# Performance work log

Measured on AMD Instinct MI355X. Metric: run time of the kernel, lower is better.

Reference implementation:

```python
import jax, jax.numpy as jnp
import numpy as np

N = 50000      # nodes
E = 800000     # edges
IN = 128       # in_channels
H = 128        # hidden_channels
OUT = 500      # out_channels
EPS = 1e-5


def setup_inputs() -> dict:
    key = jax.random.key(0)
    ks = jax.random.split(key, 8)
    def rn(k, shape, scale=0.05):
        return jax.random.normal(k, shape, jnp.float32) * scale
    return {
        "x": jax.random.normal(ks[0], (N, IN), jnp.float32),
        "edge_index": jax.random.randint(ks[1], (2, E), 0, N, dtype=jnp.int32),
        "W1": rn(ks[2], (IN, H)), "b1": jnp.zeros((H,), jnp.float32),
        "g1": jnp.ones((H,), jnp.float32), "be1": jnp.zeros((H,), jnp.float32),
        "W2": rn(ks[3], (H, 2 * H)), "b2": jnp.zeros((2 * H,), jnp.float32),
        "g2": jnp.ones((2 * H,), jnp.float32), "be2": jnp.zeros((2 * H,), jnp.float32),
        "W3": rn(ks[4], (2 * H, H)), "b3": jnp.zeros((H,), jnp.float32),
        "g3": jnp.ones((H,), jnp.float32), "be3": jnp.zeros((H,), jnp.float32),
        "Wl1": rn(ks[5], (H, H // 2)), "bl1": jnp.zeros((H // 2,), jnp.float32),
        "g4": jnp.ones((H // 2,), jnp.float32), "be4": jnp.zeros((H // 2,), jnp.float32),
        "Wl2": rn(ks[6], (H // 2, OUT)), "bl2": jnp.zeros((OUT,), jnp.float32),
    }


def layer_norm(x, g, b):
    mu = jnp.mean(x, axis=-1, keepdims=True)
    var = jnp.mean(jnp.square(x - mu), axis=-1, keepdims=True)
    return (x - mu) * jax.lax.rsqrt(var + EPS) * g + b


def gcn_conv(x, W, b, src, dst, n):
    # PyG GCNConv: x' = D^{-1/2} (A + I) D^{-1/2} (x W) + b, with self-loops.
    h = x @ W                                   # [N, F]
    ones = jnp.ones(src.shape[0], h.dtype)
    deg = jax.ops.segment_sum(ones, dst, num_segments=n) + 1.0  # +1 self-loop
    dinv = jnp.where(deg > 0, jax.lax.rsqrt(deg), 0.0)          # [N]
    coef = dinv[src] * dinv[dst]                # [E]
    agg = jax.ops.segment_sum(h[src] * coef[:, None], dst, num_segments=n)
    agg = agg + h * jnp.square(dinv)[:, None]   # self-loop messages
    return agg + b


def reference(x, edge_index, W1, b1, g1, be1, W2, b2, g2, be2,
              W3, b3, g3, be3, Wl1, bl1, g4, be4, Wl2, bl2):
    # eval mode: dropout is identity
    src, dst = edge_index[0], edge_index[1]
    n = x.shape[0]
    h = jax.nn.elu(layer_norm(gcn_conv(x, W1, b1, src, dst, n), g1, be1))
    h = jax.nn.elu(layer_norm(gcn_conv(h, W2, b2, src, dst, n), g2, be2))
    h = jax.nn.elu(layer_norm(gcn_conv(h, W3, b3, src, dst, n), g3, be3))
    h = jax.nn.elu(layer_norm(h @ Wl1 + bl1, g4, be4))
    return h @ Wl2 + bl2
```

## Files before the change

### kernel.cpp

```cpp
#include <hip/hip_runtime.h>
#include <cstdint>


#define LN_EPS 1e-5f

typedef __attribute__((ext_vector_type(8))) short bf16x8;
typedef __attribute__((ext_vector_type(4))) float f32x4;

static __device__ __forceinline__ ushort f2bf(float f) {
  union { float f; uint u; } c; c.f = f;
  uint u = c.u;
  return (ushort)((u + 0x7fffu + ((u >> 16) & 1u)) >> 16);
}
static __device__ __forceinline__ float bf2f(ushort h) {
  union { uint u; float f; } c; c.u = (uint)h << 16;
  return c.f;
}


__global__ void deg_kernel(const int* __restrict__ dst, int* __restrict__ deg, int E) {
  int e = blockIdx.x * blockDim.x + threadIdx.x;
  if (e < E) atomicAdd(&deg[dst[e]], 1);
}

__global__ void scan1_kernel(const int* __restrict__ deg, int* __restrict__ excl,
                             int* __restrict__ bsums, float* __restrict__ dinv, int N) {
  __shared__ int s[256];
  int tid = threadIdx.x;
  int i = blockIdx.x * 256 + tid;
  int v = (i < N) ? deg[i] : 0;
  s[tid] = v;
  __syncthreads();
  for (int o = 1; o < 256; o <<= 1) {
    int t = (tid >= o) ? s[tid - o] : 0;
    __syncthreads();
    if (tid >= o) s[tid] += t;
    __syncthreads();
  }
  if (i < N) {
    excl[i] = s[tid] - v;
    dinv[i] = rsqrtf((float)v + 1.0f);
  }
  if (tid == 255) bsums[blockIdx.x] = s[tid];
}

__global__ void scan23_kernel(int* __restrict__ rowptr, int* __restrict__ fill,
                              const int* __restrict__ bsums, int N, int Etotal, int nb) {
  __shared__ int sh[256];
  const int tid = threadIdx.x;
  const int bix = blockIdx.x;
  int v = (tid < bix && tid < nb) ? bsums[tid] : 0;
  sh[tid] = v;
  __syncthreads();
  for (int o = 128; o > 0; o >>= 1) {
    if (tid < o) sh[tid] += sh[tid + o];
    __syncthreads();
  }
  const int off = sh[0];
  int i = bix * 256 + tid;
  if (i < N) {
    int r = rowptr[i] + off;
    rowptr[i] = r;
    fill[i] = r;
  } else if (i == N) {
    rowptr[N] = Etotal;
  }
}

__global__ void fill_kernel(const int* __restrict__ src, const int* __restrict__ dst,
                            int* __restrict__ fill, int* __restrict__ srcs, int E) {
  int e = blockIdx.x * blockDim.x + threadIdx.x;
  if (e >= E) return;
  int idx = atomicAdd(&fill[dst[e]], 1);
  srcs[idx] = src[e];
}


struct WConvArgs {
  const float* w[5];
  ushort* wt[5];
  int K[5], N[5];
  int off[6];
};

__global__ void prep_kernel(WConvArgs a, int total, int* __restrict__ deg, int Nn) {
  int i = blockIdx.x * blockDim.x + threadIdx.x;
  if (i < Nn) deg[i] = 0;
  if (i >= total) return;
  int m = 0;
  while (i >= a.off[m + 1]) m++;
  int j = i - a.off[m];
  int k = j / a.N[m], n = j - k * a.N[m];
  a.wt[m][(size_t)n * a.K[m] + k] = f2bf(a.w[m][j]);
}

#define TBM 128
#define TBN 128
#define TBK 32
#define LDK 40

template <int AF32, int EMODE>
__global__ __launch_bounds__(256, 2) void mfma_gemm_kernel(
    const void* __restrict__ A, const ushort* __restrict__ Bt,
    const float* __restrict__ bias, const float* __restrict__ gamma,
    const float* __restrict__ beta, void* __restrict__ Cout,
    int M, int N, int K) {
  __shared__ ushort As[TBM][LDK];
  __shared__ ushort Bs[TBN][LDK];
  const int tid = threadIdx.x;
  const int lane = tid & 63;
  const int w = tid >> 6;
  const int wm = w & 1, wn = w >> 1;
  const int quad = lane >> 4, l16 = lane & 15;
  const int rowBase = blockIdx.y * TBM;
  const int colBase = blockIdx.x * TBN;

  f32x4 acc[4][4] = {};
  const int lr = tid >> 2;
  const int lk = (tid & 3) * 8;

  for (int k0 = 0; k0 < K; k0 += TBK) {
#pragma unroll
    for (int h = 0; h < 2; h++) {
      int r = lr + h * 64;
      int grow = rowBase + r;
      if (AF32) {
        const float* Af = (const float*)A;
        float4 v0 = make_float4(0.f, 0.f, 0.f, 0.f), v1 = v0;
        if (grow < M) {
          const float* ap = Af + (size_t)grow * K + k0 + lk;
          v0 = *(const float4*)ap;
          v1 = *(const float4*)(ap + 4);
        }
        uint4 wv;
        wv.x = (uint)f2bf(v0.x) | ((uint)f2bf(v0.y) << 16);
        wv.y = (uint)f2bf(v0.z) | ((uint)f2bf(v0.w) << 16);
        wv.z = (uint)f2bf(v1.x) | ((uint)f2bf(v1.y) << 16);
        wv.w = (uint)f2bf(v1.z) | ((uint)f2bf(v1.w) << 16);
        *(uint4*)&As[r][lk] = wv;
      } else {
        const ushort* Ab = (const ushort*)A;
        uint4 va = make_uint4(0, 0, 0, 0);
        if (grow < M) va = *(const uint4*)(Ab + (size_t)grow * K + k0 + lk);
        *(uint4*)&As[r][lk] = va;
      }
      int gcol = colBase + r;
      uint4 vb = make_uint4(0, 0, 0, 0);
      if (gcol < N) vb = *(const uint4*)(Bt + (size_t)gcol * K + k0 + lk);
      *(uint4*)&Bs[r][lk] = vb;
    }
    __syncthreads();
    bf16x8 af[4], bfr[4];
#pragma unroll
    for (int i = 0; i < 4; i++) {
      af[i]  = *(const bf16x8*)&As[wm * 64 + i * 16 + l16][quad * 8];
      bfr[i] = *(const bf16x8*)&Bs[wn * 64 + i * 16 + l16][quad * 8];
    }
#pragma unroll
    for (int i = 0; i < 4; i++)
#pragma unroll
      for (int j = 0; j < 4; j++)
        acc[i][j] = __builtin_amdgcn_mfma_f32_16x16x32_bf16(af[i], bfr[j], acc[i][j], 0, 0, 0);
    __syncthreads();
  }

  if constexpr (EMODE == 2) {
    if (wn != 0) return;
    const int rowB = rowBase + wm * 64;
#pragma unroll
    for (int i = 0; i < 4; i++) {
#pragma unroll
      for (int r = 0; r < 4; r++) {
        int row = rowB + i * 16 + quad * 4 + r;
        float v[4];
        float s = 0.f;
#pragma unroll
        for (int j = 0; j < 4; j++) {
          int col = j * 16 + l16;
          v[j] = acc[i][j][r] + bias[col];
          s += v[j];
        }
#pragma unroll
        for (int o = 8; o >= 1; o >>= 1) s += __shfl_xor(s, o, 16);
        float mean = s * (1.0f / 64.0f);
        float q = 0.f;
#pragma unroll
        for (int j = 0; j < 4; j++) {
          float d = v[j] - mean;
          q += d * d;
        }
#pragma unroll
        for (int o = 8; o >= 1; o >>= 1) q += __shfl_xor(q, o, 16);
        float rstd = rsqrtf(q * (1.0f / 64.0f) + LN_EPS);
        if (row < M) {
#pragma unroll
          for (int j = 0; j < 4; j++) {
            int col = j * 16 + l16;
            float y = (v[j] - mean) * rstd * gamma[col] + beta[col];
            y = (y > 0.f) ? y : expm1f(y);
            ((ushort*)Cout)[(size_t)row * 64 + col] = f2bf(y);
          }
        }
      }
    }
    return;
  } else {
#pragma unroll
    for (int i = 0; i < 4; i++) {
      int row0 = rowBase + wm * 64 + i * 16 + quad * 4;
#pragma unroll
      for (int j = 0; j < 4; j++) {
        int col = colBase + wn * 64 + j * 16 + l16;
        if (col >= N) continue;
        float bv = bias ? bias[col] : 0.f;
#pragma unroll
        for (int r = 0; r < 4; r++) {
          int row = row0 + r;
          if (row >= M) continue;
          float vv = acc[i][j][r] + bv;
          if (EMODE == 1) ((ushort*)Cout)[(size_t)row * N + col] = f2bf(vv);
          else            ((float*)Cout)[(size_t)row * N + col] = vv;
        }
      }
    }
  }
}


__global__ __launch_bounds__(256) void agg_kernel(
    const ushort* __restrict__ hb, const int* __restrict__ rowptr,
    const int* __restrict__ srcs, const float* __restrict__ dinv,
    uint* __restrict__ out, int Nn) {
  const int wave = threadIdx.x >> 6;
  const int n = blockIdx.x * 4 + wave;
  if (n >= Nn) return;
  const int f = threadIdx.x & 63;
  const uint* h32 = (const uint*)hb;
  const float di = dinv[n];
  uint self = h32[(size_t)n * 64 + f];
  float a0 = bf2f((ushort)(self & 0xffffu)) * di * di;
  float a1 = bf2f((ushort)(self >> 16)) * di * di;
  int i = rowptr[n];
  const int e = rowptr[n + 1];
  for (; i + 3 < e; i += 4) {
    int s0 = srcs[i], s1 = srcs[i + 1], s2 = srcs[i + 2], s3 = srcs[i + 3];
    float c0 = dinv[s0] * di, c1 = dinv[s1] * di, c2 = dinv[s2] * di, c3 = dinv[s3] * di;
    uint v0 = h32[(size_t)s0 * 64 + f];
    uint v1 = h32[(size_t)s1 * 64 + f];
    uint v2 = h32[(size_t)s2 * 64 + f];
    uint v3 = h32[(size_t)s3 * 64 + f];
    a0 += c0 * bf2f((ushort)(v0 & 0xffffu)) + c1 * bf2f((ushort)(v1 & 0xffffu)) +
          c2 * bf2f((ushort)(v2 & 0xffffu)) + c3 * bf2f((ushort)(v3 & 0xffffu));
    a1 += c0 * bf2f((ushort)(v0 >> 16)) + c1 * bf2f((ushort)(v1 >> 16)) +
          c2 * bf2f((ushort)(v2 >> 16)) + c3 * bf2f((ushort)(v3 >> 16));
  }
  for (; i < e; i++) {
    int s = srcs[i];
    float c = dinv[s] * di;
    uint v = h32[(size_t)s * 64 + f];
    a0 += c * bf2f((ushort)(v & 0xffffu));
    a1 += c * bf2f((ushort)(v >> 16));
  }
  out[(size_t)n * 64 + f] = (uint)f2bf(a0) | ((uint)f2bf(a1) << 16);
}

__global__ __launch_bounds__(256) void agg_ln_kernel(
    const ushort* __restrict__ hb, const int* __restrict__ rowptr,
    const int* __restrict__ srcs, const float* __restrict__ dinv,
    const float* __restrict__ bias, const float* __restrict__ g,
    const float* __restrict__ be, uint* __restrict__ out, int Nn) {
  const int wave = threadIdx.x >> 6;
  const int n = blockIdx.x * 4 + wave;
  if (n >= Nn) return;
  const int f = threadIdx.x & 63;
  const uint* h32 = (const uint*)hb;
  const float di = dinv[n];
  uint self = h32[(size_t)n * 64 + f];
  float2 bv = ((const float2*)bias)[f];
  float a0 = bf2f((ushort)(self & 0xffffu)) * di * di + bv.x;
  float a1 = bf2f((ushort)(self >> 16)) * di * di + bv.y;
  int i = rowptr[n];
  const int e = rowptr[n + 1];
  for (; i + 3 < e; i += 4) {
    int s0 = srcs[i], s1 = srcs[i + 1], s2 = srcs[i + 2], s3 = srcs[i + 3];
    float c0 = dinv[s0] * di, c1 = dinv[s1] * di, c2 = dinv[s2] * di, c3 = dinv[s3] * di;
    uint v0 = h32[(size_t)s0 * 64 + f];
    uint v1 = h32[(size_t)s1 * 64 + f];
    uint v2 = h32[(size_t)s2 * 64 + f];
    uint v3 = h32[(size_t)s3 * 64 + f];
    a0 += c0 * bf2f((ushort)(v0 & 0xffffu)) + c1 * bf2f((ushort)(v1 & 0xffffu)) +
          c2 * bf2f((ushort)(v2 & 0xffffu)) + c3 * bf2f((ushort)(v3 & 0xffffu));
    a1 += c0 * bf2f((ushort)(v0 >> 16)) + c1 * bf2f((ushort)(v1 >> 16)) +
          c2 * bf2f((ushort)(v2 >> 16)) + c3 * bf2f((ushort)(v3 >> 16));
  }
  for (; i < e; i++) {
    int s = srcs[i];
    float c = dinv[s] * di;
    uint v = h32[(size_t)s * 64 + f];
    a0 += c * bf2f((ushort)(v & 0xffffu));
    a1 += c * bf2f((ushort)(v >> 16));
  }
  float s = a0 + a1;
#pragma unroll
  for (int o = 32; o >= 1; o >>= 1) s += __shfl_xor(s, o);
  float mean = s * (1.0f / 128.0f);
  float d0 = a0 - mean, d1 = a1 - mean;
  float q = d0 * d0 + d1 * d1;
#pragma unroll
  for (int o = 32; o >= 1; o >>= 1) q += __shfl_xor(q, o);
  float rstd = rsqrtf(q * (1.0f / 128.0f) + LN_EPS);
  float2 gv = ((const float2*)g)[f];
  float2 bev = ((const float2*)be)[f];
  float y0 = d0 * rstd * gv.x + bev.x;
  float y1 = d1 * rstd * gv.y + bev.y;
  y0 = (y0 > 0.f) ? y0 : expm1f(y0);
  y1 = (y1 > 0.f) ? y1 : expm1f(y1);
  out[(size_t)n * 64 + f] = (uint)f2bf(y0) | ((uint)f2bf(y1) << 16);
}

template <int F, bool IN_BF16>
__global__ __launch_bounds__(F) void ln_elu_kernel(const void* __restrict__ xin,
                                                   const float* __restrict__ g,
                                                   const float* __restrict__ be,
                                                   ushort* __restrict__ out) {
  constexpr int NW = (F + 63) / 64;
  __shared__ float sb[NW];
  const int row = blockIdx.x;
  const int f = threadIdx.x;
  float v;
  if (IN_BF16) v = bf2f(((const ushort*)xin)[(size_t)row * F + f]);
  else         v = ((const float*)xin)[(size_t)row * F + f];
  float s = v;
#pragma unroll
  for (int o = 32; o >= 1; o >>= 1) s += __shfl_xor(s, o);
  float mean;
  if constexpr (NW == 1) {
    mean = s * (1.0f / F);
  } else {
    if ((f & 63) == 0) sb[f >> 6] = s;
    __syncthreads();
    float t = 0.f;
#pragma unroll
    for (int w2 = 0; w2 < NW; w2++) t += sb[w2];
    mean = t * (1.0f / F);
    __syncthreads();
  }
  float d = v - mean;
  float q = d * d;
#pragma unroll
  for (int o = 32; o >= 1; o >>= 1) q += __shfl_xor(q, o);
  float var;
  if constexpr (NW == 1) {
    var = q * (1.0f / F);
  } else {
    if ((f & 63) == 0) sb[f >> 6] = q;
    __syncthreads();
    float t = 0.f;
#pragma unroll
    for (int w2 = 0; w2 < NW; w2++) t += sb[w2];
    var = t * (1.0f / F);
  }
  float y = d * rsqrtf(var + LN_EPS) * g[f] + be[f];
  out[(size_t)row * F + f] = f2bf((y > 0.f) ? y : expm1f(y));
}


extern "C" void kernel_launch(void* const* d_in, const int* in_sizes, int n_in,
                              void* d_out, int out_size, void* d_ws, size_t ws_size,
                              hipStream_t stream) {
  const float* x   = (const float*)d_in[0];
  const int*   ei  = (const int*)d_in[1];
  const float* W1  = (const float*)d_in[2];
  const float* b1  = (const float*)d_in[3];
  const float* g1  = (const float*)d_in[4];
  const float* be1 = (const float*)d_in[5];
  const float* W2  = (const float*)d_in[6];
  const float* b2  = (const float*)d_in[7];
  const float* g2  = (const float*)d_in[8];
  const float* be2 = (const float*)d_in[9];
  const float* W3  = (const float*)d_in[10];
  const float* b3  = (const float*)d_in[11];
  const float* g3  = (const float*)d_in[12];
  const float* be3 = (const float*)d_in[13];
  const float* Wl1 = (const float*)d_in[14];
  const float* bl1 = (const float*)d_in[15];
  const float* g4  = (const float*)d_in[16];
  const float* be4 = (const float*)d_in[17];
  const float* Wl2 = (const float*)d_in[18];
  const float* bl2 = (const float*)d_in[19];

  const int N = in_sizes[0] / 128;
  const int E = in_sizes[1] / 2;
  const int* esrc = ei;
  const int* edst = ei + E;

  char* p = (char*)d_ws;
  ushort* Pb = (ushort*)p;            p += (size_t)N * 256 * 2;
  ushort* Qb = (ushort*)p;            p += (size_t)N * 256 * 2;
  ushort* W1t = (ushort*)p;           p += 128 * 128 * 2;
  ushort* W2t = (ushort*)p;           p += 128 * 256 * 2;
  ushort* W3t = (ushort*)p;           p += 256 * 128 * 2;
  ushort* Wl1t = (ushort*)p;          p += 128 * 64 * 2;
  ushort* Wl2t = (ushort*)p;          p += 64 * 500 * 2;
  int*   srcs  = (int*)p;             p += (size_t)E * 4;
  int*   deg   = (int*)p;             p += (size_t)N * 4;
  float* dinv  = (float*)p;           p += (size_t)N * 4;
  int*   rowptr= (int*)p;             p += (size_t)(N + 2) * 4;
  int*   fill  = (int*)p;             p += (size_t)N * 4;
  int*   bsums = (int*)p;             p += 256 * 4;

  const int nb = (N + 255) / 256;
  const int eb = (E + 255) / 256;

  WConvArgs wa;
  wa.w[0] = W1;  wa.wt[0] = W1t;  wa.K[0] = 128; wa.N[0] = 128;
  wa.w[1] = W2;  wa.wt[1] = W2t;  wa.K[1] = 128; wa.N[1] = 256;
  wa.w[2] = W3;  wa.wt[2] = W3t;  wa.K[2] = 256; wa.N[2] = 128;
  wa.w[3] = Wl1; wa.wt[3] = Wl1t; wa.K[3] = 128; wa.N[3] = 64;
  wa.w[4] = Wl2; wa.wt[4] = Wl2t; wa.K[4] = 64;  wa.N[4] = 500;
  wa.off[0] = 0;
  for (int m = 0; m < 5; m++) wa.off[m + 1] = wa.off[m] + wa.K[m] * wa.N[m];
  int wtotal = wa.off[5];
  int ptotal = wtotal > N ? wtotal : N;
  prep_kernel<<<(ptotal + 255) / 256, 256, 0, stream>>>(wa, wtotal, deg, N);

  deg_kernel<<<eb, 256, 0, stream>>>(edst, deg, E);
  scan1_kernel<<<nb, 256, 0, stream>>>(deg, rowptr, bsums, dinv, N);
  scan23_kernel<<<(N + 256) / 256, 256, 0, stream>>>(rowptr, fill, bsums, N, E, nb);
  fill_kernel<<<eb, 256, 0, stream>>>(esrc, edst, fill, srcs, E);

  const int ab = (N + 3) / 4;
  auto grid_of = [&](int M, int Nn) {
    return dim3((Nn + TBN - 1) / TBN, (M + TBM - 1) / TBM);
  };

  mfma_gemm_kernel<1, 1><<<grid_of(N, 128), 256, 0, stream>>>(
      x, W1t, nullptr, nullptr, nullptr, Pb, N, 128, 128);
  agg_ln_kernel<<<ab, 256, 0, stream>>>(Pb, rowptr, srcs, dinv, b1, g1, be1, (uint*)Qb, N);

  agg_kernel<<<ab, 256, 0, stream>>>(Qb, rowptr, srcs, dinv, (uint*)Pb, N);
  mfma_gemm_kernel<0, 1><<<grid_of(N, 256), 256, 0, stream>>>(
      Pb, W2t, b2, nullptr, nullptr, Qb, N, 256, 128);
  ln_elu_kernel<256, true><<<N, 256, 0, stream>>>(Qb, g2, be2, Pb);

  mfma_gemm_kernel<0, 1><<<grid_of(N, 128), 256, 0, stream>>>(
      Pb, W3t, nullptr, nullptr, nullptr, Qb, N, 128, 256);
  agg_ln_kernel<<<ab, 256, 0, stream>>>(Qb, rowptr, srcs, dinv, b3, g3, be3, (uint*)Pb, N);

  mfma_gemm_kernel<0, 2><<<grid_of(N, 64), 256, 0, stream>>>(
      Pb, Wl1t, bl1, g4, be4, Qb, N, 64, 128);

  mfma_gemm_kernel<0, 0><<<grid_of(N, 500), 256, 0, stream>>>(
      Qb, Wl2t, bl2, nullptr, nullptr, d_out, N, 500, 64);
}
```

Measured before the change: 518.7 us.

## Vectorize GCN aggregation with 16-byte gathers and 4 edges per wave

Restructures the aggregation kernels so each wave splits into four 16-lane groups. Each lane loads a uint4 (8 bf16 features), so the wave processes four neighbor rows in parallel, and the partial sums are combined across groups with cross-lane shuffles. The aim is fewer, wider memory transactions and more gathers in flight per wave to hide latency in this gather-bound step. The cost is extra accumulator registers, shuffle-reduction work, and idle lanes during the output/LayerNorm epilogue. Separately, the fp32 GEMM output path now uses nontemporal stores.

```diff
diff --git a/kernel.cpp b/kernel.cpp
--- a/kernel.cpp
+++ b/kernel.cpp
@@ -219,13 +219,20 @@
           if (row >= M) continue;
           float vv = acc[i][j][r] + bv;
           if (EMODE == 1) ((ushort*)Cout)[(size_t)row * N + col] = f2bf(vv);
-          else            ((float*)Cout)[(size_t)row * N + col] = vv;
+          else __builtin_nontemporal_store(vv, &((float*)Cout)[(size_t)row * N + col]);
         }
       }
     }
   }
 }
 
+
+static __device__ __forceinline__ void acc8(float* a, uint4 v, float c) {
+  a[0] += c * bf2f((ushort)(v.x & 0xffffu)); a[1] += c * bf2f((ushort)(v.x >> 16));
+  a[2] += c * bf2f((ushort)(v.y & 0xffffu)); a[3] += c * bf2f((ushort)(v.y >> 16));
+  a[4] += c * bf2f((ushort)(v.z & 0xffffu)); a[5] += c * bf2f((ushort)(v.z >> 16));
+  a[6] += c * bf2f((ushort)(v.w & 0xffffu)); a[7] += c * bf2f((ushort)(v.w >> 16));
+}
 
 __global__ __launch_bounds__(256) void agg_kernel(
     const ushort* __restrict__ hb, const int* __restrict__ rowptr,
@@ -234,88 +241,125 @@
   const int wave = threadIdx.x >> 6;
   const int n = blockIdx.x * 4 + wave;
   if (n >= Nn) return;
-  const int f = threadIdx.x & 63;
-  const uint* h32 = (const uint*)hb;
+  const int lane = threadIdx.x & 63;
+  const int g = lane >> 4, l16 = lane & 15;
+  const uint4* h4 = (const uint4*)hb;
   const float di = dinv[n];
-  uint self = h32[(size_t)n * 64 + f];
-  float a0 = bf2f((ushort)(self & 0xffffu)) * di * di;
-  float a1 = bf2f((ushort)(self >> 16)) * di * di;
-  int i = rowptr[n];
+  float a[8] = {0.f, 0.f, 0.f, 0.f, 0.f, 0.f, 0.f, 0.f};
+  if (g == 0) {
+    uint4 sv = h4[(size_t)n * 16 + l16];
+    acc8(a, sv, di * di);
+  }
+  int i = rowptr[n] + g;
   const int e = rowptr[n + 1];
-  for (; i + 3 < e; i += 4) {
-    int s0 = srcs[i], s1 = srcs[i + 1], s2 = srcs[i + 2], s3 = srcs[i + 3];
-    float c0 = dinv[s0] * di, c1 = dinv[s1] * di, c2 = dinv[s2] * di, c3 = dinv[s3] * di;
-    uint v0 = h32[(size_t)s0 * 64 + f];
-    uint v1 = h32[(size_t)s1 * 64 + f];
-    uint v2 = h32[(size_t)s2 * 64 + f];
-    uint v3 = h32[(size_t)s3 * 64 + f];
-    a0 += c0 * bf2f((ushort)(v0 & 0xffffu)) + c1 * bf2f((ushort)(v1 & 0xffffu)) +
-          c2 * bf2f((ushort)(v2 & 0xffffu)) + c3 * bf2f((ushort)(v3 & 0xffffu));
-    a1 += c0 * bf2f((ushort)(v0 >> 16)) + c1 * bf2f((ushort)(v1 >> 16)) +
-          c2 * bf2f((ushort)(v2 >> 16)) + c3 * bf2f((ushort)(v3 >> 16));
-  }
-  for (; i < e; i++) {
+  for (; i + 4 < e; i += 8) {
+    int s0 = srcs[i], s1 = srcs[i + 4];
+    float c0 = dinv[s0] * di, c1 = dinv[s1] * di;
+    uint4 v0 = h4[(size_t)s0 * 16 + l16];
+    uint4 v1 = h4[(size_t)s1 * 16 + l16];
+    acc8(a, v0, c0);
+    acc8(a, v1, c1);
+  }
+  if (i < e) {
     int s = srcs[i];
     float c = dinv[s] * di;
-    uint v = h32[(size_t)s * 64 + f];
-    a0 += c * bf2f((ushort)(v & 0xffffu));
-    a1 += c * bf2f((ushort)(v >> 16));
-  }
-  out[(size_t)n * 64 + f] = (uint)f2bf(a0) | ((uint)f2bf(a1) << 16);
+    uint4 v = h4[(size_t)s * 16 + l16];
+    acc8(a, v, c);
+  }
+#pragma unroll
+  for (int k = 0; k < 8; k++) {
+    a[k] += __shfl_xor(a[k], 16);
+    a[k] += __shfl_xor(a[k], 32);
+  }
+  if (g == 0) {
+    uint4 o;
+    o.x = (uint)f2bf(a[0]) | ((uint)f2bf(a[1]) << 16);
+    o.y = (uint)f2bf(a[2]) | ((uint)f2bf(a[3]) << 16);
+    o.z = (uint)f2bf(a[4]) | ((uint)f2bf(a[5]) << 16);
+    o.w = (uint)f2bf(a[6]) | ((uint)f2bf(a[7]) << 16);
+    ((uint4*)out)[(size_t)n * 16 + l16] = o;
+  }
 }
 
 __global__ __launch_bounds__(256) void agg_ln_kernel(
     const ushort* __restrict__ hb, const int* __restrict__ rowptr,
     const int* __restrict__ srcs, const float* __restrict__ dinv,
-    const float* __restrict__ bias, const float* __restrict__ g,
-    const float* __restrict__ be, uint* __restrict__ out, int Nn) {
+    const float* __restrict__ bias, const float* __restrict__ gamma,
+    const float* __restrict__ beta, uint* __restrict__ out, int Nn) {
   const int wave = threadIdx.x >> 6;
   const int n = blockIdx.x * 4 + wave;
   if (n >= Nn) return;
-  const int f = threadIdx.x & 63;
-  const uint* h32 = (const uint*)hb;
+  const int lane = threadIdx.x & 63;
+  const int g = lane >> 4, l16 = lane & 15;
+  const uint4* h4 = (const uint4*)hb;
   const float di = dinv[n];
-  uint self = h32[(size_t)n * 64 + f];
-  float2 bv = ((const float2*)bias)[f];
-  float a0 = bf2f((ushort)(self & 0xffffu)) * di * di + bv.x;
-  float a1 = bf2f((ushort)(self >> 16)) * di * di + bv.y;
-  int i = rowptr[n];
+  float a[8] = {0.f, 0.f, 0.f, 0.f, 0.f, 0.f, 0.f, 0.f};
+  if (g == 0) {
+    uint4 sv = h4[(size_t)n * 16 + l16];
+    acc8(a, sv, di * di);
+    float4 b0 = ((const float4*)bias)[l16 * 2];
+    float4 b1 = ((const float4*)bias)[l16 * 2 + 1];
+    a[0] += b0.x; a[1] += b0.y; a[2] += b0.z; a[3] += b0.w;
+    a[4] += b1.x; a[5] += b1.y; a[6] += b1.z; a[7] += b1.w;
+  }
+  int i = rowptr[n] + g;
   const int e = rowptr[n + 1];
-  for (; i + 3 < e; i += 4) {
-    int s0 = srcs[i], s1 = srcs[i + 1], s2 = srcs[i + 2], s3 = srcs[i + 3];
-    float c0 = dinv[s0] * di, c1 = dinv[s1] * di, c2 = dinv[s2] * di, c3 = dinv[s3] * di;
-    uint v0 = h32[(size_t)s0 * 64 + f];
-    uint v1 = h32[(size_t)s1 * 64 + f];
-    uint v2 = h32[(size_t)s2 * 64 + f];
-    uint v3 = h32[(size_t)s3 * 64 + f];
-    a0 += c0 * bf2f((ushort)(v0 & 0xffffu)) + c1 * bf2f((ushort)(v1 & 0xffffu)) +
-          c2 * bf2f((ushort)(v2 & 0xffffu)) + c3 * bf2f((ushort)(v3 & 0xffffu));
-    a1 += c0 * bf2f((ushort)(v0 >> 16)) + c1 * bf2f((ushort)(v1 >> 16)) +
-          c2 * bf2f((ushort)(v2 >> 16)) + c3 * bf2f((ushort)(v3 >> 16));
-  }
-  for (; i < e; i++) {
+  for (; i + 4 < e; i += 8) {
+    int s0 = srcs[i], s1 = srcs[i + 4];
+    float c0 = dinv[s0] * di, c1 = dinv[s1] * di;
+    uint4 v0 = h4[(size_t)s0 * 16 + l16];
+    uint4 v1 = h4[(size_t)s1 * 16 + l16];
+    acc8(a, v0, c0);
+    acc8(a, v1, c1);
+  }
+  if (i < e) {
     int s = srcs[i];
     float c = dinv[s] * di;
-    uint v = h32[(size_t)s * 64 + f];
-    a0 += c * bf2f((ushort)(v & 0xffffu));
-    a1 += c * bf2f((ushort)(v >> 16));
-  }
-  float s = a0 + a1;
-#pragma unroll
-  for (int o = 32; o >= 1; o >>= 1) s += __shfl_xor(s, o);
+    uint4 v = h4[(size_t)s * 16 + l16];
+    acc8(a, v, c);
+  }
+#pragma unroll
+  for (int k = 0; k < 8; k++) {
+    a[k] += __shfl_xor(a[k], 16);
+    a[k] += __shfl_xor(a[k], 32);
+  }
+  float s = ((a[0] + a[1]) + (a[2] + a[3])) + ((a[4] + a[5]) + (a[6] + a[7]));
+  s += __shfl_xor(s, 8);
+  s += __shfl_xor(s, 4);
+  s += __shfl_xor(s, 2);
+  s += __shfl_xor(s, 1);
   float mean = s * (1.0f / 128.0f);
-  float d0 = a0 - mean, d1 = a1 - mean;
-  float q = d0 * d0 + d1 * d1;
-#pragma unroll
-  for (int o = 32; o >= 1; o >>= 1) q += __shfl_xor(q, o);
+  float q = 0.f;
+#pragma unroll
+  for (int k = 0; k < 8; k++) {
+    float d = a[k] - mean;
+    q += d * d;
+  }
+  q += __shfl_xor(q, 8);
+  q += __shfl_xor(q, 4);
+  q += __shfl_xor(q, 2);
+  q += __shfl_xor(q, 1);
   float rstd = rsqrtf(q * (1.0f / 128.0f) + LN_EPS);
-  float2 gv = ((const float2*)g)[f];
-  float2 bev = ((const float2*)be)[f];
-  float y0 = d0 * rstd * gv.x + bev.x;
-  float y1 = d1 * rstd * gv.y + bev.y;
-  y0 = (y0 > 0.f) ? y0 : expm1f(y0);
-  y1 = (y1 > 0.f) ? y1 : expm1f(y1);
-  out[(size_t)n * 64 + f] = (uint)f2bf(y0) | ((uint)f2bf(y1) << 16);
+  if (g == 0) {
+    float4 g0 = ((const float4*)gamma)[l16 * 2];
+    float4 g1 = ((const float4*)gamma)[l16 * 2 + 1];
+    float4 e0 = ((const float4*)beta)[l16 * 2];
+    float4 e1 = ((const float4*)beta)[l16 * 2 + 1];
+    float gv[8] = {g0.x, g0.y, g0.z, g0.w, g1.x, g1.y, g1.z, g1.w};
+    float ev[8] = {e0.x, e0.y, e0.z, e0.w, e1.x, e1.y, e1.z, e1.w};
+    float y[8];
+#pragma unroll
+    for (int k = 0; k < 8; k++) {
+      float t = (a[k] - mean) * rstd * gv[k] + ev[k];
+      y[k] = (t > 0.f) ? t : expm1f(t);
+    }
+    uint4 o;
+    o.x = (uint)f2bf(y[0]) | ((uint)f2bf(y[1]) << 16);
+    o.y = (uint)f2bf(y[2]) | ((uint)f2bf(y[3]) << 16);
+    o.z = (uint)f2bf(y[4]) | ((uint)f2bf(y[5]) << 16);
+    o.w = (uint)f2bf(y[6]) | ((uint)f2bf(y[7]) << 16);
+    ((uint4*)out)[(size_t)n * 16 + l16] = o;
+  }
 }
 
 template <int F, bool IN_BF16>
```

New measurement: 580.7 us. 1.12x slower.
